# Kernel tuning notes

Hardware: AMD Instinct MI355X
Metric: run time of the kernel (lower is better)

The kernel has to match this reference:

```python
import jax, jax.numpy as jnp
import numpy as np

N, IN, OUT = 128, 1024, 1024
STE_TEMP = 1.0


def setup_inputs() -> dict:
    key = jax.random.key(0)
    k1, k2 = jax.random.split(key)
    x = jax.random.normal(k1, (N, IN), dtype=jnp.float32)
    # nn.init.uniform_(weight, -0.5, 0.5)
    weight = jax.random.uniform(k2, (OUT, IN), dtype=jnp.float32, minval=-0.5, maxval=0.5)
    bias = jnp.zeros((OUT,), dtype=jnp.float32)
    return {"x": x, "weight": weight, "bias": bias}


def reference(x, weight, bias):
    # scores: [N, out, in] = W[out,in] broadcast-added to x[N,1,in]
    scores = weight[None, :, :] + x[:, None, :]
    # training-mode forward: hard max value, STE blend with softmax-weighted smooth value
    hard = jnp.max(jax.lax.stop_gradient(scores), axis=-1)          # [N, out]
    soft_w = jax.nn.softmax(scores / STE_TEMP, axis=-1)              # [N, out, in]
    soft = jnp.sum(soft_w * scores, axis=-1)                          # [N, out]
    out = hard + (soft - jax.lax.stop_gradient(soft))
    return out + bias
```

## Files before the change

### kernel.cpp

```cpp
#include <hip/hip_runtime.h>

#define N_ROWS 128
#define IN_DIM 1024
#define OUT_DIM 1024


__global__ __launch_bounds__(256, 2)
void tropical_linear_kernel(const float* __restrict__ x,
                            const float* __restrict__ w,
                            const float* __restrict__ bias,
                            float* __restrict__ out) {
    __shared__ float4 xs[4 * 256];

    const int tid  = threadIdx.x;
    const int wid  = tid >> 6;
    const int lane = tid & 63;
    const int g    = lane & 15;
    const int og   = lane >> 4;

    const int bn = blockIdx.x >> 4;
    const int bo = blockIdx.x & 15;
    const int n0 = bn * 4;
    const int obase = bo * 64 + wid * 16 + og * 4;

    const float4* __restrict__ x4 = (const float4*)x;

    const float4* __restrict__ wp0 = (const float4*)w + (size_t)(obase + 0) * 256 + g;
    const float4* __restrict__ wp1 = (const float4*)w + (size_t)(obase + 1) * 256 + g;
    const float4* __restrict__ wp2 = (const float4*)w + (size_t)(obase + 2) * 256 + g;
    const float4* __restrict__ wp3 = (const float4*)w + (size_t)(obase + 3) * 256 + g;

#pragma unroll
    for (int i = 0; i < 4; ++i) {
        const int idx = tid + i * 256;
        xs[idx] = x4[(size_t)(n0 + (idx >> 8)) * 256 + (idx & 255)];
    }

    float4 wA[4], wB[4];
    wA[0] = wp0[0];  wA[1] = wp1[0];  wA[2] = wp2[0];  wA[3] = wp3[0];
    wB[0] = wp0[16]; wB[1] = wp1[16]; wB[2] = wp2[16]; wB[3] = wp3[16];

    float acc[4][4];
#pragma unroll
    for (int j = 0; j < 4; ++j)
#pragma unroll
        for (int r = 0; r < 4; ++r) acc[j][r] = -3.4e38f;

    __syncthreads();

    const float4* __restrict__ xsg = xs + g;

    float4 xA[4], xB[4];
#pragma unroll
    for (int j = 0; j < 4; ++j) xA[j] = xsg[j * 256];

#define TROPIC_STEP(WBUF, XBUF)                                   \
    _Pragma("unroll")                                             \
    for (int j = 0; j < 4; ++j) {                                 \
        const float4 xv = XBUF[j];                                \
        _Pragma("unroll")                                         \
        for (int r = 0; r < 4; ++r) {                             \
            const float s0 = WBUF[r].x + xv.x;                    \
            const float s1 = WBUF[r].y + xv.y;                    \
            const float s2 = WBUF[r].z + xv.z;                    \
            const float s3 = WBUF[r].w + xv.w;                    \
            const float m = fmaxf(fmaxf(s0, s1), s2);             \
            acc[j][r] = fmaxf(fmaxf(m, s3), acc[j][r]);           \
        }                                                         \
    }

#pragma unroll 1
    for (int tt = 0; tt < 7; ++tt) {
        const int t0 = 2 * tt;
#pragma unroll
        for (int j = 0; j < 4; ++j) xB[j] = xsg[j * 256 + (t0 + 1) * 16];
        TROPIC_STEP(wA, xA)
        wA[0] = wp0[(t0 + 2) * 16]; wA[1] = wp1[(t0 + 2) * 16];
        wA[2] = wp2[(t0 + 2) * 16]; wA[3] = wp3[(t0 + 2) * 16];
#pragma unroll
        for (int j = 0; j < 4; ++j) xA[j] = xsg[j * 256 + (t0 + 2) * 16];
        TROPIC_STEP(wB, xB)
        wB[0] = wp0[(t0 + 3) * 16]; wB[1] = wp1[(t0 + 3) * 16];
        wB[2] = wp2[(t0 + 3) * 16]; wB[3] = wp3[(t0 + 3) * 16];
    }
#pragma unroll
    for (int j = 0; j < 4; ++j) xB[j] = xsg[j * 256 + 15 * 16];
    TROPIC_STEP(wA, xA)
    TROPIC_STEP(wB, xB)

#undef TROPIC_STEP

#pragma unroll
    for (int j = 0; j < 4; ++j) {
#pragma unroll
        for (int r = 0; r < 4; ++r) {
            float v = acc[j][r];
            v = fmaxf(v, __shfl_xor(v, 1, 64));
            v = fmaxf(v, __shfl_xor(v, 2, 64));
            v = fmaxf(v, __shfl_xor(v, 4, 64));
            v = fmaxf(v, __shfl_xor(v, 8, 64));
            acc[j][r] = v;
        }
    }

    if (g < 8) {
        const int jj = g & 3;
        const int pr = (g >> 2) & 1;
        float2 res = make_float2(0.f, 0.f);
#pragma unroll
        for (int j = 0; j < 4; ++j) {
            if (jj == j) {
                res.x = pr ? acc[j][2] : acc[j][0];
                res.y = pr ? acc[j][3] : acc[j][1];
            }
        }
        const int oc = obase + pr * 2;
        const float2 bv = *(const float2*)&bias[oc];
        res.x += bv.x;
        res.y += bv.y;
        *(float2*)&out[(size_t)(n0 + jj) * OUT_DIM + oc] = res;
    }
}

extern "C" void kernel_launch(void* const* d_in, const int* in_sizes, int n_in,
                              void* d_out, int out_size, void* d_ws, size_t ws_size,
                              hipStream_t stream) {
    const float* x    = (const float*)d_in[0];
    const float* w    = (const float*)d_in[1];
    const float* bias = (const float*)d_in[2];
    float* out = (float*)d_out;

    dim3 grid(512);
    dim3 block(256);
    hipLaunchKernelGGL(tropical_linear_kernel, grid, block, 0, stream, x, w, bias, out);
}
```

Measured before the change: 72.14 us.

## Stage weight tile in LDS, keep x in registers, reduce via LDS transpose

Retiles each block to 16 rows by 16 outputs, loading the 16 weight rows into shared memory and each wave's 4 x rows into registers, so each thread accumulates 64 partial maxima over its slice of the inner dimension. The cross-lane max reduction is replaced with a padded shared-memory transpose followed by a per-lane serial reduction. This increases register reuse per LDS read but loses the previous overlap of global weight loads with compute and uses much more LDS and registers, which may reduce occupancy.

```diff
diff --git a/kernel.cpp b/kernel.cpp
--- a/kernel.cpp
+++ b/kernel.cpp
@@ -10,116 +10,85 @@
                             const float* __restrict__ w,
                             const float* __restrict__ bias,
                             float* __restrict__ out) {
-    __shared__ float4 xs[4 * 256];
+    __shared__ float lds_raw[4 * 64 * 65];
+    float4* wlds = (float4*)lds_raw;
 
     const int tid  = threadIdx.x;
     const int wid  = tid >> 6;
     const int lane = tid & 63;
-    const int g    = lane & 15;
-    const int og   = lane >> 4;
 
-    const int bn = blockIdx.x >> 4;
-    const int bo = blockIdx.x & 15;
-    const int n0 = bn * 4;
-    const int obase = bo * 64 + wid * 16 + og * 4;
+    const int bn = blockIdx.x >> 6;
+    const int bo = blockIdx.x & 63;
+    const int n0 = bn * 16;
+    const int o0 = bo * 16;
 
-    const float4* __restrict__ x4 = (const float4*)x;
-
-    const float4* __restrict__ wp0 = (const float4*)w + (size_t)(obase + 0) * 256 + g;
-    const float4* __restrict__ wp1 = (const float4*)w + (size_t)(obase + 1) * 256 + g;
-    const float4* __restrict__ wp2 = (const float4*)w + (size_t)(obase + 2) * 256 + g;
-    const float4* __restrict__ wp3 = (const float4*)w + (size_t)(obase + 3) * 256 + g;
-
+    const float4* __restrict__ wg = (const float4*)w + (size_t)o0 * 256;
 #pragma unroll
-    for (int i = 0; i < 4; ++i) {
+    for (int i = 0; i < 16; ++i) {
         const int idx = tid + i * 256;
-        xs[idx] = x4[(size_t)(n0 + (idx >> 8)) * 256 + (idx & 255)];
+        wlds[idx] = wg[idx];
     }
 
-    float4 wA[4], wB[4];
-    wA[0] = wp0[0];  wA[1] = wp1[0];  wA[2] = wp2[0];  wA[3] = wp3[0];
-    wB[0] = wp0[16]; wB[1] = wp1[16]; wB[2] = wp2[16]; wB[3] = wp3[16];
-
-    float acc[4][4];
+    const float4* __restrict__ xg =
+        (const float4*)x + (size_t)(n0 + wid * 4) * 256 + lane;
+    float4 xr[4][4];
 #pragma unroll
     for (int j = 0; j < 4; ++j)
 #pragma unroll
-        for (int r = 0; r < 4; ++r) acc[j][r] = -3.4e38f;
+        for (int s = 0; s < 4; ++s)
+            xr[j][s] = xg[j * 256 + s * 64];
+
+    float acc[4][16];
+#pragma unroll
+    for (int j = 0; j < 4; ++j)
+#pragma unroll
+        for (int o = 0; o < 16; ++o) acc[j][o] = -3.4e38f;
 
     __syncthreads();
 
-    const float4* __restrict__ xsg = xs + g;
-
-    float4 xA[4], xB[4];
+    const float4* __restrict__ wl = wlds + lane;
 #pragma unroll
-    for (int j = 0; j < 4; ++j) xA[j] = xsg[j * 256];
-
-#define TROPIC_STEP(WBUF, XBUF)                                   \
-    _Pragma("unroll")                                             \
-    for (int j = 0; j < 4; ++j) {                                 \
-        const float4 xv = XBUF[j];                                \
-        _Pragma("unroll")                                         \
-        for (int r = 0; r < 4; ++r) {                             \
-            const float s0 = WBUF[r].x + xv.x;                    \
-            const float s1 = WBUF[r].y + xv.y;                    \
-            const float s2 = WBUF[r].z + xv.z;                    \
-            const float s3 = WBUF[r].w + xv.w;                    \
-            const float m = fmaxf(fmaxf(s0, s1), s2);             \
-            acc[j][r] = fmaxf(fmaxf(m, s3), acc[j][r]);           \
-        }                                                         \
+    for (int o = 0; o < 16; ++o) {
+        float4 wv[4];
+#pragma unroll
+        for (int s = 0; s < 4; ++s) wv[s] = wl[o * 256 + s * 64];
+#pragma unroll
+        for (int j = 0; j < 4; ++j)
+#pragma unroll
+            for (int s = 0; s < 4; ++s) {
+                const float4 xv = xr[j][s];
+                const float s0 = wv[s].x + xv.x;
+                const float s1 = wv[s].y + xv.y;
+                const float s2 = wv[s].z + xv.z;
+                const float s3 = wv[s].w + xv.w;
+                const float m = fmaxf(fmaxf(s0, s1), s2);
+                acc[j][o] = fmaxf(fmaxf(m, s3), acc[j][o]);
+            }
     }
 
-#pragma unroll 1
-    for (int tt = 0; tt < 7; ++tt) {
-        const int t0 = 2 * tt;
-#pragma unroll
-        for (int j = 0; j < 4; ++j) xB[j] = xsg[j * 256 + (t0 + 1) * 16];
-        TROPIC_STEP(wA, xA)
-        wA[0] = wp0[(t0 + 2) * 16]; wA[1] = wp1[(t0 + 2) * 16];
-        wA[2] = wp2[(t0 + 2) * 16]; wA[3] = wp3[(t0 + 2) * 16];
-#pragma unroll
-        for (int j = 0; j < 4; ++j) xA[j] = xsg[j * 256 + (t0 + 2) * 16];
-        TROPIC_STEP(wB, xB)
-        wB[0] = wp0[(t0 + 3) * 16]; wB[1] = wp1[(t0 + 3) * 16];
-        wB[2] = wp2[(t0 + 3) * 16]; wB[3] = wp3[(t0 + 3) * 16];
-    }
-#pragma unroll
-    for (int j = 0; j < 4; ++j) xB[j] = xsg[j * 256 + 15 * 16];
-    TROPIC_STEP(wA, xA)
-    TROPIC_STEP(wB, xB)
-
-#undef TROPIC_STEP
+    __syncthreads();
+    float* scr = lds_raw + wid * (64 * 65);
 
 #pragma unroll
-    for (int j = 0; j < 4; ++j) {
+    for (int j = 0; j < 4; ++j)
 #pragma unroll
-        for (int r = 0; r < 4; ++r) {
-            float v = acc[j][r];
-            v = fmaxf(v, __shfl_xor(v, 1, 64));
-            v = fmaxf(v, __shfl_xor(v, 2, 64));
-            v = fmaxf(v, __shfl_xor(v, 4, 64));
-            v = fmaxf(v, __shfl_xor(v, 8, 64));
-            acc[j][r] = v;
-        }
+        for (int o = 0; o < 16; ++o)
+            scr[(j * 16 + o) * 65 + lane] = acc[j][o];
+
+    const float* scrp = scr + lane * 65;
+    float m0 = -3.4e38f, m1 = -3.4e38f, m2 = -3.4e38f, m3 = -3.4e38f;
+#pragma unroll
+    for (int l = 0; l < 16; ++l) {
+        m0 = fmaxf(m0, scrp[4 * l + 0]);
+        m1 = fmaxf(m1, scrp[4 * l + 1]);
+        m2 = fmaxf(m2, scrp[4 * l + 2]);
+        m3 = fmaxf(m3, scrp[4 * l + 3]);
     }
+    const float m = fmaxf(fmaxf(m0, m1), fmaxf(m2, m3));
 
-    if (g < 8) {
-        const int jj = g & 3;
-        const int pr = (g >> 2) & 1;
-        float2 res = make_float2(0.f, 0.f);
-#pragma unroll
-        for (int j = 0; j < 4; ++j) {
-            if (jj == j) {
-                res.x = pr ? acc[j][2] : acc[j][0];
-                res.y = pr ? acc[j][3] : acc[j][1];
-            }
-        }
-        const int oc = obase + pr * 2;
-        const float2 bv = *(const float2*)&bias[oc];
-        res.x += bv.x;
-        res.y += bv.y;
-        *(float2*)&out[(size_t)(n0 + jj) * OUT_DIM + oc] = res;
-    }
+    const int j = lane >> 4;
+    const int o = lane & 15;
+    out[(size_t)(n0 + wid * 4 + j) * OUT_DIM + o0 + o] = m + bias[o0 + o];
 }
 
 extern "C" void kernel_launch(void* const* d_in, const int* in_sizes, int n_in,
@@ -132,5 +101,6 @@
 
     dim3 grid(512);
     dim3 block(256);
-    hipLaunchKernelGGL(tropical_linear_kernel, grid, block, 0, stream, x, w, bias, out);
+    hipLaunchKernelGGL(tropical_linear_kernel, grid, block, 0, stream,
+                       x, w, bias, out);
 }
```

Result: faster. 66.04 us (-8.5%).
